# Kernel optimization log

Measured on AMD Instinct MI355X. Metric: run time of the kernel, lower is better.

Reference implementation:

```python
import math
import jax, jax.numpy as jnp
import numpy as np

BATCH, SEQ, D_MODEL, D_STATE = 2, 2048, 1024, 16
PROJ = 2 * D_MODEL + 2 * D_MODEL * D_STATE


def setup_inputs() -> dict:
    key = jax.random.key(0)
    kx, kw = jax.random.split(key)
    x = jax.random.normal(kx, (BATCH, SEQ, D_MODEL), dtype=jnp.float32)
    # in_proj: xavier_uniform weight, zero bias
    bound = math.sqrt(6.0 / (D_MODEL + PROJ))
    W = jax.random.uniform(kw, (PROJ, D_MODEL), jnp.float32, -bound, bound)
    b = jnp.zeros((PROJ,), jnp.float32)
    # A init: -exp(log(1000) * s/d_state), repeated over d_model
    dl = jnp.arange(D_STATE, dtype=jnp.float32) / D_STATE
    A = jnp.broadcast_to(-jnp.exp(math.log(1000.0) * dl), (D_MODEL, D_STATE)).astype(jnp.float32)
    D = jnp.ones((D_MODEL,), jnp.float32)
    return {"x": x, "W": W, "b": b, "A": A, "D": D}


def reference(x, W, b, A, D):
    bsz, seq, dm = x.shape
    ds = A.shape[1]
    # in_proj
    xp = jnp.einsum('bsd,pd->bsp', x, W) + b
    u, delta, Bp, Cp = jnp.split(xp, [dm, 2 * dm, 2 * dm + dm * ds], axis=-1)
    delta = jax.nn.softplus(delta)                       # (b,s,d)
    Bm = Bp.reshape(bsz, seq, dm, ds)                    # (b,s,d,n)
    Cm = Cp.reshape(bsz, seq, dm, ds)
    Abar = jnp.exp(A * delta[..., None])                 # (b,s,d,n)

    def step(h, inp):
        Abar_t, B_t, C_t, u_t = inp                      # (b,d,n),(b,d,n),(b,d,n),(b,d)
        h = Abar_t * h + B_t * u_t[..., None]
        y_t = jnp.sum(C_t * h, axis=-1)                  # (b,d)
        return h, y_t

    h0 = jnp.zeros((bsz, dm, ds), dtype=x.dtype)
    xs = (jnp.swapaxes(Abar, 0, 1), jnp.swapaxes(Bm, 0, 1),
          jnp.swapaxes(Cm, 0, 1), jnp.swapaxes(u, 0, 1))
    _, ys = jax.lax.scan(step, h0, xs)                   # ys: (s,b,d)
    y = jnp.swapaxes(ys, 0, 1) + D * u                   # skip connection
    return y  # dropout=0.0 -> identity
```

## Files before the change

### kernel.cpp

```cpp
#include <hip/hip_runtime.h>
#include <hip/hip_bf16.h>
#include <stdint.h>

#define BATCH 2
#define SEQ   2048
#define DM    1024
#define DS    16
#define PROJ  34816
#define MTOK  4096
#define KDIM  1024
#define NCHUNK 16
#define CHUNK  128
#define NCH    32768

typedef unsigned short u16;
typedef unsigned int   u32;
typedef __attribute__((ext_vector_type(8))) __bf16 bf16x8;
typedef __attribute__((ext_vector_type(4))) float  f32x4;

__device__ __forceinline__ float ldf(const float* p) { return *p; }
__device__ __forceinline__ float ldf(const __hip_bfloat16* p) { return __bfloat162float(*p); }
__device__ __forceinline__ void stf(float* p, float v) { *p = v; }
__device__ __forceinline__ void stf(__hip_bfloat16* p, float v) { *p = __float2bfloat16(v); }

__device__ __forceinline__ void gl16(const void* g, void* l) {
  __builtin_amdgcn_global_load_lds(
      (const __attribute__((address_space(1))) u32*)g,
      (__attribute__((address_space(3))) u32*)(u32)(uintptr_t)l,
      16, 0, 0);
}

__device__ __forceinline__ f32x4 mfma16(bf16x8 a, bf16x8 b, f32x4 c) {
  return __builtin_amdgcn_mfma_f32_16x16x32_bf16(a, b, c, 0, 0, 0);
}

__global__ __launch_bounds__(256)
void split_kernel(const float* __restrict__ src, u16* __restrict__ hi,
                  u16* __restrict__ lo, int n4) {
  int i = blockIdx.x * 256 + threadIdx.x;
  if (i >= n4) return;
  float4 v = reinterpret_cast<const float4*>(src)[i];
  ushort4 h, l;
  {
    __hip_bfloat16 bh, bl;
    bh = __float2bfloat16(v.x); bl = __float2bfloat16(v.x - __bfloat162float(bh));
    h.x = *(u16*)&bh; l.x = *(u16*)&bl;
    bh = __float2bfloat16(v.y); bl = __float2bfloat16(v.y - __bfloat162float(bh));
    h.y = *(u16*)&bh; l.y = *(u16*)&bl;
    bh = __float2bfloat16(v.z); bl = __float2bfloat16(v.z - __bfloat162float(bh));
    h.z = *(u16*)&bh; l.z = *(u16*)&bl;
    bh = __float2bfloat16(v.w); bl = __float2bfloat16(v.w - __bfloat162float(bh));
    h.w = *(u16*)&bh; l.w = *(u16*)&bl;
  }
  reinterpret_cast<ushort4*>(hi)[i] = h;
  reinterpret_cast<ushort4*>(lo)[i] = l;
}

#define BM 128
#define BN 128
#define BK 32

template <typename OutT>
__global__ __launch_bounds__(256, 2)
void gemm_kernel(const u16* __restrict__ xHi, const u16* __restrict__ xLo,
                 const u16* __restrict__ wHi, const u16* __restrict__ wLo,
                 const float* __restrict__ bias, OutT* __restrict__ xp) {
  __shared__ __align__(16) u16 sAh[BM * BK];
  __shared__ __align__(16) u16 sAl[BM * BK];
  __shared__ __align__(16) u16 sBh[BN * BK];
  __shared__ __align__(16) u16 sBl[BN * BK];

  const int tid  = threadIdx.x;
  const int lane = tid & 63;
  const int wid  = tid >> 6;
  const int wr   = wid >> 1;
  const int wc   = wid & 1;

  const int bid = blockIdx.x;
  const int mt  = bid & 31;
  const int nt  = bid >> 5;
  const int m0  = mt * BM;
  const int n0  = nt * BN;

  const int srow = tid >> 2;
  const int scol = (tid & 3) * 8;
  const u16* gAh = xHi + (size_t)(m0 + srow) * KDIM + scol;
  const u16* gAl = xLo + (size_t)(m0 + srow) * KDIM + scol;
  const u16* gBh = wHi + (size_t)(n0 + srow) * KDIM + scol;
  const u16* gBl = wLo + (size_t)(n0 + srow) * KDIM + scol;
  u16* lAh = sAh + tid * 8;
  u16* lAl = sAl + tid * 8;
  u16* lBh = sBh + tid * 8;
  u16* lBl = sBl + tid * 8;

  f32x4 acc[4][4] = {};

  const int fr = lane & 15;
  const int kq = (lane >> 4) * 8;

  for (int kt = 0; kt < KDIM / BK; ++kt) {
    const int k0 = kt * BK;
    gl16(gAh + k0, lAh);  gl16(gAh + 64 * KDIM + k0, lAh + 64 * BK);
    gl16(gAl + k0, lAl);  gl16(gAl + 64 * KDIM + k0, lAl + 64 * BK);
    gl16(gBh + k0, lBh);  gl16(gBh + 64 * KDIM + k0, lBh + 64 * BK);
    gl16(gBl + k0, lBl);  gl16(gBl + 64 * KDIM + k0, lBl + 64 * BK);
    __syncthreads();

    bf16x8 ah[4], al[4], bh[4], bl[4];
#pragma unroll
    for (int i = 0; i < 4; ++i) {
      ah[i] = *(const bf16x8*)&sAh[(wr * 64 + i * 16 + fr) * BK + kq];
      al[i] = *(const bf16x8*)&sAl[(wr * 64 + i * 16 + fr) * BK + kq];
      bh[i] = *(const bf16x8*)&sBh[(wc * 64 + i * 16 + fr) * BK + kq];
      bl[i] = *(const bf16x8*)&sBl[(wc * 64 + i * 16 + fr) * BK + kq];
    }
#pragma unroll
    for (int mi = 0; mi < 4; ++mi)
#pragma unroll
      for (int ni = 0; ni < 4; ++ni) {
        acc[mi][ni] = mfma16(ah[mi], bh[ni], acc[mi][ni]);
        acc[mi][ni] = mfma16(ah[mi], bl[ni], acc[mi][ni]);
        acc[mi][ni] = mfma16(al[mi], bh[ni], acc[mi][ni]);
      }
    __syncthreads();
  }

  const int rq = (lane >> 4) * 4;
#pragma unroll
  for (int mi = 0; mi < 4; ++mi) {
#pragma unroll
    for (int ni = 0; ni < 4; ++ni) {
      const int col = n0 + wc * 64 + ni * 16 + fr;
      const float bv = bias[col];
      const bool isdelta = (col >= DM) && (col < 2 * DM);
      const int row = m0 + wr * 64 + mi * 16 + rq;
#pragma unroll
      for (int j = 0; j < 4; ++j) {
        float v = acc[mi][ni][j] + bv;
        if (isdelta) v = (v > 20.f) ? v : log1pf(__expf(v));
        stf(&xp[(size_t)(row + j) * PROJ + col], v);
      }
    }
  }
}

template <typename InT>
__global__ __launch_bounds__(256)
void scan_phase1(const InT* __restrict__ xp, const float* __restrict__ A,
                 float* __restrict__ P, float* __restrict__ Hl) {
  const int bidx = blockIdx.x;
  const int c  = bidx & 15;
  const int dt = (bidx >> 4) & 63;
  const int b  = bidx >> 10;
  const int tid = threadIdx.x;
  const int n  = tid & 15;
  const int dl = tid >> 4;
  const int d  = dt * 16 + dl;

  const float Ad = A[d * DS + n];
  const size_t row0 = ((size_t)(b * SEQ) + c * CHUNK) * PROJ;
  const InT* pu = xp + row0 + d;
  const InT* pq = xp + row0 + DM + d;
  const InT* pB = xp + row0 + 2 * DM + d * DS + n;

  float p = 1.f, h = 0.f;
  for (int t = 0; t < CHUNK; ++t) {
    float u  = ldf(pu);
    float dq = ldf(pq);
    float Bv = ldf(pB);
    float a  = __expf(Ad * dq);
    h = a * h + Bv * u;
    p *= a;
    pu += PROJ; pq += PROJ; pB += PROJ;
  }
  const int ch = ((b * DM + d) * DS + n);
  P[(size_t)c * NCH + ch]  = p;
  Hl[(size_t)c * NCH + ch] = h;
}

__global__ __launch_bounds__(256)
void scan_phase2(const float* __restrict__ P, const float* __restrict__ Hl,
                 float* __restrict__ Hst) {
  const int ch = blockIdx.x * 256 + threadIdx.x;
  float h = 0.f;
  for (int c = 0; c < NCHUNK; ++c) {
    Hst[(size_t)c * NCH + ch] = h;
    h = P[(size_t)c * NCH + ch] * h + Hl[(size_t)c * NCH + ch];
  }
}

template <typename InT>
__global__ __launch_bounds__(256)
void scan_phase3(const InT* __restrict__ xp, const float* __restrict__ A,
                 const float* __restrict__ Dv, const float* __restrict__ Hst,
                 float* __restrict__ y) {
  const int bidx = blockIdx.x;
  const int c  = bidx & 15;
  const int dt = (bidx >> 4) & 63;
  const int b  = bidx >> 10;
  const int tid = threadIdx.x;
  const int n  = tid & 15;
  const int dl = tid >> 4;
  const int d  = dt * 16 + dl;

  const float Ad = A[d * DS + n];
  const float Dd = Dv[d];
  const int ch = ((b * DM + d) * DS + n);
  float h = Hst[(size_t)c * NCH + ch];

  const int t0 = c * CHUNK;
  const size_t row0 = ((size_t)(b * SEQ) + t0) * PROJ;
  const InT* pu = xp + row0 + d;
  const InT* pq = xp + row0 + DM + d;
  const InT* pB = xp + row0 + 2 * DM + d * DS + n;
  const InT* pC = pB + DM * DS;
  float* py = y + ((size_t)(b * SEQ) + t0) * DM + d;

  for (int t = 0; t < CHUNK; ++t) {
    float u  = ldf(pu);
    float dq = ldf(pq);
    float Bv = ldf(pB);
    float Cv = ldf(pC);
    float a  = __expf(Ad * dq);
    h = a * h + Bv * u;
    float ph = Cv * h;
    ph += __shfl_xor(ph, 1);
    ph += __shfl_xor(ph, 2);
    ph += __shfl_xor(ph, 4);
    ph += __shfl_xor(ph, 8);
    if (n == 0) *py = ph + Dd * u;
    pu += PROJ; pq += PROJ; pB += PROJ; pC += PROJ; py += DM;
  }
}

extern "C" void kernel_launch(void* const* d_in, const int* in_sizes, int n_in,
                              void* d_out, int out_size, void* d_ws, size_t ws_size,
                              hipStream_t stream) {
  const float* x  = (const float*)d_in[0];
  const float* W  = (const float*)d_in[1];
  const float* b  = (const float*)d_in[2];
  const float* A  = (const float*)d_in[3];
  const float* Dv = (const float*)d_in[4];
  float* y = (float*)d_out;

  char* ws = (char*)d_ws;
  size_t off = 0;
  auto alloc = [&](size_t bytes) {
    void* p = ws + off;
    off += (bytes + 255) & ~(size_t)255;
    return p;
  };

  u16* xHi = (u16*)alloc((size_t)MTOK * KDIM * sizeof(u16));
  u16* xLo = (u16*)alloc((size_t)MTOK * KDIM * sizeof(u16));
  u16* wHi = (u16*)alloc((size_t)PROJ * KDIM * sizeof(u16));
  u16* wLo = (u16*)alloc((size_t)PROJ * KDIM * sizeof(u16));
  float* P   = (float*)alloc((size_t)NCHUNK * NCH * sizeof(float));
  float* Hl  = (float*)alloc((size_t)NCHUNK * NCH * sizeof(float));
  float* Hst = (float*)alloc((size_t)NCHUNK * NCH * sizeof(float));
  const size_t xp_elems = (size_t)MTOK * PROJ;
  const bool xp_f32 = ws_size >= off + xp_elems * sizeof(float);
  void* xp = alloc(xp_elems * (xp_f32 ? sizeof(float) : sizeof(__hip_bfloat16)));

  split_kernel<<<(MTOK * KDIM / 4 + 255) / 256, 256, 0, stream>>>(x, xHi, xLo, MTOK * KDIM / 4);
  split_kernel<<<(PROJ * KDIM / 4 + 255) / 256, 256, 0, stream>>>(W, wHi, wLo, PROJ * KDIM / 4);

  const int gemm_grid = (MTOK / BM) * (PROJ / BN);
  const int scan_grid = BATCH * 64 * NCHUNK;

  if (xp_f32) {
    float* xpf = (float*)xp;
    gemm_kernel<float><<<gemm_grid, 256, 0, stream>>>(xHi, xLo, wHi, wLo, b, xpf);
    scan_phase1<float><<<scan_grid, 256, 0, stream>>>(xpf, A, P, Hl);
    scan_phase2<<<NCH / 256, 256, 0, stream>>>(P, Hl, Hst);
    scan_phase3<float><<<scan_grid, 256, 0, stream>>>(xpf, A, Dv, Hst, y);
  } else {
    __hip_bfloat16* xpb = (__hip_bfloat16*)xp;
    gemm_kernel<__hip_bfloat16><<<gemm_grid, 256, 0, stream>>>(xHi, xLo, wHi, wLo, b, xpb);
    scan_phase1<__hip_bfloat16><<<scan_grid, 256, 0, stream>>>(xpb, A, P, Hl);
    scan_phase2<<<NCH / 256, 256, 0, stream>>>(P, Hl, Hst);
    scan_phase3<__hip_bfloat16><<<scan_grid, 256, 0, stream>>>(xpb, A, Dv, Hst, y);
  }
}
```

Measured before the change: 1.171 ms.

## Enlarge GEMM tiles to 256x256 with double-buffered swizzled LDS and XCD remap

Rewrites the split-bf16 GEMM to use 256x256 tiles with 512 threads, interleaving hi/lo halves in one XOR-swizzled LDS buffer and double-buffering global-to-LDS loads so the next K-slice loads while MFMAs run. It also remaps block IDs across the 8 XCDs to improve L2 locality, and raises MFMA priority with s_setprio. The aim is more reuse per loaded byte, fewer barriers, and fewer LDS bank conflicts. The cost is 128KB of LDS and many more accumulator registers per thread, which may limit occupancy. The launch-bounds hint of 2 blocks may not be achievable at that LDS size.

```diff
diff --git a/kernel.cpp b/kernel.cpp
--- a/kernel.cpp
+++ b/kernel.cpp
@@ -56,87 +56,122 @@
   reinterpret_cast<ushort4*>(lo)[i] = l;
 }
 
-#define BM 128
-#define BN 128
+#define BM 256
+#define BN 256
 #define BK 32
+#define KT (KDIM / BK)
 
 template <typename OutT>
-__global__ __launch_bounds__(256, 2)
+__global__ __launch_bounds__(512, 2)
 void gemm_kernel(const u16* __restrict__ xHi, const u16* __restrict__ xLo,
                  const u16* __restrict__ wHi, const u16* __restrict__ wLo,
                  const float* __restrict__ bias, OutT* __restrict__ xp) {
-  __shared__ __align__(16) u16 sAh[BM * BK];
-  __shared__ __align__(16) u16 sAl[BM * BK];
-  __shared__ __align__(16) u16 sBh[BN * BK];
-  __shared__ __align__(16) u16 sBl[BN * BK];
+  __shared__ __align__(16) u16 sA0[16384];
+  __shared__ __align__(16) u16 sB0[16384];
+  __shared__ __align__(16) u16 sA1[16384];
+  __shared__ __align__(16) u16 sB1[16384];
 
   const int tid  = threadIdx.x;
   const int lane = tid & 63;
   const int wid  = tid >> 6;
-  const int wr   = wid >> 1;
-  const int wc   = wid & 1;
+  const int wr   = wid >> 2;
+  const int wc   = wid & 3;
+  const int fr   = lane & 15;
 
   const int bid = blockIdx.x;
-  const int mt  = bid & 31;
-  const int nt  = bid >> 5;
+  const int wg  = (bid & 7) * 272 + (bid >> 3);
+  const int mt  = wg & 15;
+  const int nt  = wg >> 4;
   const int m0  = mt * BM;
   const int n0  = nt * BN;
 
-  const int srow = tid >> 2;
-  const int scol = (tid & 3) * 8;
-  const u16* gAh = xHi + (size_t)(m0 + srow) * KDIM + scol;
-  const u16* gAl = xLo + (size_t)(m0 + srow) * KDIM + scol;
-  const u16* gBh = wHi + (size_t)(n0 + srow) * KDIM + scol;
-  const u16* gBl = wLo + (size_t)(n0 + srow) * KDIM + scol;
-  u16* lAh = sAh + tid * 8;
-  u16* lAl = sAl + tid * 8;
-  u16* lBh = sBh + tid * 8;
-  u16* lBl = sBl + tid * 8;
-
-  f32x4 acc[4][4] = {};
-
-  const int fr = lane & 15;
-  const int kq = (lane >> 4) * 8;
-
-  for (int kt = 0; kt < KDIM / BK; ++kt) {
-    const int k0 = kt * BK;
-    gl16(gAh + k0, lAh);  gl16(gAh + 64 * KDIM + k0, lAh + 64 * BK);
-    gl16(gAl + k0, lAl);  gl16(gAl + 64 * KDIM + k0, lAl + 64 * BK);
-    gl16(gBh + k0, lBh);  gl16(gBh + 64 * KDIM + k0, lBh + 64 * BK);
-    gl16(gBl + k0, lBl);  gl16(gBl + 64 * KDIM + k0, lBl + 64 * BK);
-    __syncthreads();
-
-    bf16x8 ah[4], al[4], bh[4], bl[4];
-#pragma unroll
-    for (int i = 0; i < 4; ++i) {
-      ah[i] = *(const bf16x8*)&sAh[(wr * 64 + i * 16 + fr) * BK + kq];
-      al[i] = *(const bf16x8*)&sAl[(wr * 64 + i * 16 + fr) * BK + kq];
-      bh[i] = *(const bf16x8*)&sBh[(wc * 64 + i * 16 + fr) * BK + kq];
-      bl[i] = *(const bf16x8*)&sBl[(wc * 64 + i * 16 + fr) * BK + kq];
-    }
-#pragma unroll
-    for (int mi = 0; mi < 4; ++mi)
-#pragma unroll
-      for (int ni = 0; ni < 4; ++ni) {
-        acc[mi][ni] = mfma16(ah[mi], bh[ni], acc[mi][ni]);
-        acc[mi][ni] = mfma16(ah[mi], bl[ni], acc[mi][ni]);
-        acc[mi][ni] = mfma16(al[mi], bh[ni], acc[mi][ni]);
+  const u16* srcA[4];
+  const u16* srcB[4];
+#pragma unroll
+  for (int j = 0; j < 4; ++j) {
+    const u32 p = (u32)tid * 16u + (u32)j * 8192u;
+    const u32 q = p ^ (((p >> 7) & 7u) << 4);
+    const int row  = (int)(q >> 7);
+    const int half = (int)((q >> 6) & 1u);
+    const int koff = (int)(q & 63u) >> 1;
+    srcA[j] = (half ? xLo : xHi) + (size_t)(m0 + row) * KDIM + koff;
+    srcB[j] = (half ? wLo : wHi) + (size_t)(n0 + row) * KDIM + koff;
+  }
+
+  const int inner = (((lane >> 4) * 16) ^ ((lane & 7) << 4));
+  int aOff[8], bOff[4];
+#pragma unroll
+  for (int mi = 0; mi < 8; ++mi)
+    aOff[mi] = (wr * 128 + mi * 16 + fr) * 128 + inner;
+#pragma unroll
+  for (int nj = 0; nj < 4; ++nj)
+    bOff[nj] = (wc * 64 + nj * 16 + fr) * 128 + inner;
+
+  f32x4 acc[8][4] = {};
+
+  auto stage = [&](u16* sAn, u16* sBn) {
+#pragma unroll
+    for (int j = 0; j < 4; ++j) {
+      gl16(srcA[j], (char*)sAn + tid * 16 + j * 8192);
+      srcA[j] += BK;
+    }
+#pragma unroll
+    for (int j = 0; j < 4; ++j) {
+      gl16(srcB[j], (char*)sBn + tid * 16 + j * 8192);
+      srcB[j] += BK;
+    }
+  };
+
+  auto step = [&](const u16* sAc, const u16* sBc, u16* sAn, u16* sBn,
+                  bool doStage) {
+    if (doStage) stage(sAn, sBn);
+    const char* cA = (const char*)sAc;
+    const char* cB = (const char*)sBc;
+    bf16x8 bh[4], bl[4];
+#pragma unroll
+    for (int nj = 0; nj < 4; ++nj) {
+      bh[nj] = *(const bf16x8*)(cB + bOff[nj]);
+      bl[nj] = *(const bf16x8*)(cB + (bOff[nj] ^ 64));
+    }
+    __builtin_amdgcn_s_setprio(1);
+#pragma unroll
+    for (int mi = 0; mi < 8; ++mi) {
+      bf16x8 ah = *(const bf16x8*)(cA + aOff[mi]);
+      bf16x8 al = *(const bf16x8*)(cA + (aOff[mi] ^ 64));
+#pragma unroll
+      for (int nj = 0; nj < 4; ++nj) {
+        acc[mi][nj] = mfma16(ah, bh[nj], acc[mi][nj]);
+        acc[mi][nj] = mfma16(ah, bl[nj], acc[mi][nj]);
+        acc[mi][nj] = mfma16(al, bh[nj], acc[mi][nj]);
       }
-    __syncthreads();
+    }
+    __builtin_amdgcn_s_setprio(0);
+    asm volatile("s_waitcnt vmcnt(0) lgkmcnt(0)" ::: "memory");
+    __builtin_amdgcn_s_barrier();
+  };
+
+  stage(sA0, sB0);
+  asm volatile("s_waitcnt vmcnt(0) lgkmcnt(0)" ::: "memory");
+  __builtin_amdgcn_s_barrier();
+
+#pragma unroll 1
+  for (int t = 0; t < KT / 2; ++t) {
+    step(sA0, sB0, sA1, sB1, true);
+    step(sA1, sB1, sA0, sB0, t < KT / 2 - 1);
   }
 
   const int rq = (lane >> 4) * 4;
 #pragma unroll
-  for (int mi = 0; mi < 4; ++mi) {
-#pragma unroll
-    for (int ni = 0; ni < 4; ++ni) {
-      const int col = n0 + wc * 64 + ni * 16 + fr;
+  for (int mi = 0; mi < 8; ++mi) {
+#pragma unroll
+    for (int nj = 0; nj < 4; ++nj) {
+      const int col = n0 + wc * 64 + nj * 16 + fr;
       const float bv = bias[col];
       const bool isdelta = (col >= DM) && (col < 2 * DM);
-      const int row = m0 + wr * 64 + mi * 16 + rq;
+      const int row = m0 + wr * 128 + mi * 16 + rq;
 #pragma unroll
       for (int j = 0; j < 4; ++j) {
-        float v = acc[mi][ni][j] + bv;
+        float v = acc[mi][nj][j] + bv;
         if (isdelta) v = (v > 20.f) ? v : log1pf(__expf(v));
         stf(&xp[(size_t)(row + j) * PROJ + col], v);
       }
@@ -270,13 +305,13 @@
 
   if (xp_f32) {
     float* xpf = (float*)xp;
-    gemm_kernel<float><<<gemm_grid, 256, 0, stream>>>(xHi, xLo, wHi, wLo, b, xpf);
+    gemm_kernel<float><<<gemm_grid, 512, 0, stream>>>(xHi, xLo, wHi, wLo, b, xpf);
     scan_phase1<float><<<scan_grid, 256, 0, stream>>>(xpf, A, P, Hl);
     scan_phase2<<<NCH / 256, 256, 0, stream>>>(P, Hl, Hst);
     scan_phase3<float><<<scan_grid, 256, 0, stream>>>(xpf, A, Dv, Hst, y);
   } else {
     __hip_bfloat16* xpb = (__hip_bfloat16*)xp;
-    gemm_kernel<__hip_bfloat16><<<gemm_grid, 256, 0, stream>>>(xHi, xLo, wHi, wLo, b, xpb);
+    gemm_kernel<__hip_bfloat16><<<gemm_grid, 512, 0, stream>>>(xHi, xLo, wHi, wLo, b, xpb);
     scan_phase1<__hip_bfloat16><<<scan_grid, 256, 0, stream>>>(xpb, A, P, Hl);
     scan_phase2<<<NCH / 256, 256, 0, stream>>>(P, Hl, Hst);
     scan_phase3<__hip_bfloat16><<<scan_grid, 256, 0, stream>>>(xpb, A, Dv, Hst, y);
```

Result: slower. 1.341 ms (+14.5%).
